# Kernel optimization log

Hardware: AMD Instinct MI355X
Metric: run time of the kernel (lower is better)

Reference implementation:

```python
import jax, jax.numpy as jnp
import numpy as np

LATENT = 1024
ENC = 4096
B = 8192


def setup_inputs() -> dict:
    key = jax.random.key(0)
    k1, k2, k3, k4 = jax.random.split(key, 4)
    inp = jax.random.normal(k1, (B, LATENT), dtype=jnp.float32)
    enc = jax.random.normal(k2, (B, ENC), dtype=jnp.float32)
    # nn.Linear(ENC, LATENT): weight [LATENT, ENC], bias [LATENT]
    bound = 1.0 / np.sqrt(ENC)
    W = jax.random.uniform(k3, (LATENT, ENC), minval=-bound, maxval=bound, dtype=jnp.float32)
    b = jax.random.uniform(k4, (LATENT,), minval=-bound, maxval=bound, dtype=jnp.float32)
    return {"input": inp, "encoder_output": enc, "W": W, "b": b}


def reference(input, encoder_output, W, b):
    # vector = Linear(encoder_output)  -> [B, LATENT]
    v = jnp.einsum("be,de->bd", encoder_output, W) + b
    # Fused Householder-style reflection (math identical to bmm(vv^T, x)):
    # out = x - 2 * v * (v . x) / ||v||   (original divides by norm, not norm^2)
    dot = jnp.sum(v * input, axis=1, keepdims=True)          # [B, 1]
    norm = jnp.linalg.norm(v, axis=1, keepdims=True)         # [B, 1]
    output = input - 2.0 * v * dot / norm                    # [B, LATENT]
    log_det = jnp.zeros((input.shape[0], 1), dtype=input.dtype)
    return (output, log_det)
```

## Files before the change

kernel.cpp:

```cpp
#include <hip/hip_runtime.h>
#include <hip/hip_bf16.h>
#include <stdint.h>

#define M_DIM 8192
#define N_DIM 1024
#define K_DIM 4096

typedef __bf16 bf16x8 __attribute__((ext_vector_type(8)));
typedef float f32x4 __attribute__((ext_vector_type(4)));
typedef __hip_bfloat16 bf16_t;
typedef f32x4 AccT[2][4][2][2];

__device__ __forceinline__ void gload_lds16(const void* g, void* l) {
  __builtin_amdgcn_global_load_lds(
      (const __attribute__((address_space(1))) void*)g,
      (__attribute__((address_space(3))) void*)l, 16, 0, 0);
}

__global__ __launch_bounds__(256) void pack_swz(const float* __restrict__ src,
                                                int4* __restrict__ dst) {
  const unsigned tid = blockIdx.x * 256 + threadIdx.x;
  const unsigned cp = tid & 7;
  const unsigned tmp = tid >> 3;
  const unsigned r = tmp & 255;
  const unsigned tmp2 = tmp >> 8;
  const unsigned kt = tmp2 & 63;
  const unsigned rt = tmp2 >> 6;
  const unsigned srow = (rt << 8) + r;
  const unsigned k0 = (kt << 6) + ((cp ^ (r & 7)) << 3);
  const float4* s = (const float4*)(src + (size_t)srow * 4096 + k0);
  float4 a = s[0], b = s[1];
  union { bf16_t h[8]; int4 v; } u;
  u.h[0] = __float2bfloat16(a.x); u.h[1] = __float2bfloat16(a.y);
  u.h[2] = __float2bfloat16(a.z); u.h[3] = __float2bfloat16(a.w);
  u.h[4] = __float2bfloat16(b.x); u.h[5] = __float2bfloat16(b.y);
  u.h[6] = __float2bfloat16(b.z); u.h[7] = __float2bfloat16(b.w);
  dst[tid] = u.v;
}

__device__ __forceinline__ void stage_half(const char* g, char* smem, int ldsoff, int tid) {
  gload_lds16(g + tid * 16, smem + ldsoff + tid * 16);
  gload_lds16(g + 8192 + tid * 16, smem + ldsoff + 8192 + tid * 16);
}

template <int QM, int QN, int VM>
__device__ __forceinline__ void phase(char* smem, int bb, int wm, int wn,
                                      int lrow, int lkc, int tid,
                                      const char* gsrc, int ldsoff, AccT& acc) {
  bf16x8 af[4][2];
  bf16x8 bfr[2][2];
  const char* ab = smem + bb * 65536;
  #pragma unroll
  for (int f = 0; f < 4; ++f)
    #pragma unroll
    for (int s = 0; s < 2; ++s) {
      int r = QM * 128 + wm * 64 + f * 16 + lrow;
      int c = s * 4 + lkc;
      af[f][s] = *(const bf16x8*)(ab + r * 128 + ((c ^ (r & 7)) << 4));
    }
  #pragma unroll
  for (int f2 = 0; f2 < 2; ++f2)
    #pragma unroll
    for (int s = 0; s < 2; ++s) {
      int r = QN * 128 + wn * 32 + f2 * 16 + lrow;
      int c = s * 4 + lkc;
      bfr[f2][s] = *(const bf16x8*)(ab + 32768 + r * 128 + ((c ^ (r & 7)) << 4));
    }
  stage_half(gsrc, smem, ldsoff, tid);
  __builtin_amdgcn_sched_barrier(0);
  __builtin_amdgcn_s_barrier();
  asm volatile("s_waitcnt lgkmcnt(0)" ::: "memory");
  __builtin_amdgcn_sched_barrier(0);
  __builtin_amdgcn_s_setprio(1);
  #pragma unroll
  for (int f = 0; f < 4; ++f)
    #pragma unroll
    for (int f2 = 0; f2 < 2; ++f2)
      #pragma unroll
      for (int s = 0; s < 2; ++s)
        acc[QM][f][QN][f2] = __builtin_amdgcn_mfma_f32_16x16x32_bf16(
            af[f][s], bfr[f2][s], acc[QM][f][QN][f2], 0, 0, 0);
  __builtin_amdgcn_s_setprio(0);
  if constexpr (VM == 10) asm volatile("s_waitcnt vmcnt(10)" ::: "memory");
  if constexpr (VM == 4)  asm volatile("s_waitcnt vmcnt(4)" ::: "memory");
  __builtin_amdgcn_sched_barrier(0);
  __builtin_amdgcn_s_barrier();
}

__global__ __launch_bounds__(512, 2) void gemm8(
    const char* __restrict__ pA, const char* __restrict__ pB,
    float* __restrict__ V0, float* __restrict__ V1p, int NT) {
  extern __shared__ char smem[];
  const int tid = threadIdx.x;
  const int lane = tid & 63, wave = tid >> 6;
  const int wm = wave >> 2, wn = wave & 3;
  const int lrow = lane & 15, lkc = lane >> 4;

  const int cpx = (int)gridDim.x >> 3;
  const int swz = ((int)blockIdx.x & 7) * cpx + ((int)blockIdx.x >> 3);
  const int split = swz >> 7;
  const int rem = swz & 127;
  const int mt = rem >> 2, nt = rem & 3;

  const char* Abase = pA + ((size_t)mt * 64 + (size_t)split * NT) * 32768;
  const char* Bbase = pB + ((size_t)nt * 64 + (size_t)split * NT) * 32768;
  float* V = split ? V1p : V0;

  AccT acc;
  #pragma unroll
  for (int a0 = 0; a0 < 2; ++a0)
    #pragma unroll
    for (int a1 = 0; a1 < 4; ++a1)
      #pragma unroll
      for (int a2 = 0; a2 < 2; ++a2)
        #pragma unroll
        for (int a3 = 0; a3 < 2; ++a3)
          acc[a0][a1][a2][a3] = (f32x4){0.f, 0.f, 0.f, 0.f};

  const int ktm = NT - 1;

  stage_half(Abase, smem, 0, tid);
  stage_half(Bbase + 16384, smem, 32768 + 16384, tid);
  stage_half(Abase + 16384, smem, 16384, tid);
  stage_half(Bbase, smem, 32768, tid);
  stage_half(Abase + 32768, smem, 65536, tid);
  stage_half(Bbase + 32768 + 16384, smem, 65536 + 32768 + 16384, tid);
  asm volatile("s_waitcnt vmcnt(4)" ::: "memory");
  __builtin_amdgcn_s_barrier();

  for (int g = 0; g < NT; ++g) {
    const int bb = g & 1, nbf = bb ^ 1;
    const char* A1t = Abase + (size_t)((g + 1) & ktm) * 32768;
    const char* B1t = Bbase + (size_t)((g + 1) & ktm) * 32768;
    const char* A2t = Abase + (size_t)((g + 2) & ktm) * 32768;
    const char* B2t = Bbase + (size_t)((g + 2) & ktm) * 32768;
    phase<0, 0, 0>(smem, bb, wm, wn, lrow, lkc, tid, A1t + 16384, nbf * 65536 + 16384, acc);
    phase<0, 1, 10>(smem, bb, wm, wn, lrow, lkc, tid, B1t, nbf * 65536 + 32768, acc);
    phase<1, 1, 0>(smem, bb, wm, wn, lrow, lkc, tid, A2t, bb * 65536, acc);
    phase<1, 0, 4>(smem, bb, wm, wn, lrow, lkc, tid, B2t + 16384, bb * 65536 + 32768 + 16384, acc);
  }

  const int lq = lane >> 4;
  #pragma unroll
  for (int qm = 0; qm < 2; ++qm)
    #pragma unroll
    for (int f = 0; f < 4; ++f)
      #pragma unroll
      for (int qn = 0; qn < 2; ++qn)
        #pragma unroll
        for (int f2 = 0; f2 < 2; ++f2) {
          const int rowg = mt * 256 + qm * 128 + wm * 64 + f * 16 + lq * 4;
          const int colg = nt * 256 + qn * 128 + wn * 32 + f2 * 16 + lrow;
          #pragma unroll
          for (int reg = 0; reg < 4; ++reg)
            V[(size_t)(rowg + reg) * N_DIM + colg] = acc[qm][f][qn][f2][reg];
        }
}

__global__ __launch_bounds__(256) void householder_ep(
    const float* __restrict__ x, const float* __restrict__ bias,
    float* __restrict__ vio, const float* __restrict__ V2,
    float* __restrict__ logdet) {
  const int row = blockIdx.x;
  const int t = threadIdx.x;
  float4* vr = (float4*)(vio + (size_t)row * N_DIM);
  const float4* xr = (const float4*)(x + (size_t)row * N_DIM);
  const float4* br = (const float4*)bias;

  float4 v = vr[t];
  if (V2) {
    float4 v2 = ((const float4*)(V2 + (size_t)row * N_DIM))[t];
    v.x += v2.x; v.y += v2.y; v.z += v2.z; v.w += v2.w;
  }
  float4 bb = br[t];
  v.x += bb.x; v.y += bb.y; v.z += bb.z; v.w += bb.w;
  float4 xx = xr[t];

  float dot = v.x * xx.x + v.y * xx.y + v.z * xx.z + v.w * xx.w;
  float nsq = v.x * v.x + v.y * v.y + v.z * v.z + v.w * v.w;

  #pragma unroll
  for (int off = 32; off > 0; off >>= 1) {
    dot += __shfl_down(dot, off);
    nsq += __shfl_down(nsq, off);
  }
  __shared__ float sd[4], sn[4];
  if ((t & 63) == 0) { sd[t >> 6] = dot; sn[t >> 6] = nsq; }
  __syncthreads();
  dot = sd[0] + sd[1] + sd[2] + sd[3];
  nsq = sn[0] + sn[1] + sn[2] + sn[3];

  const float f = 2.0f * dot / sqrtf(nsq);
  float4 o;
  o.x = xx.x - f * v.x;
  o.y = xx.y - f * v.y;
  o.z = xx.z - f * v.z;
  o.w = xx.w - f * v.w;
  vr[t] = o;
  if (t == 0) logdet[row] = 0.0f;
}

extern "C" void kernel_launch(void* const* d_in, const int* in_sizes, int n_in,
                              void* d_out, int out_size, void* d_ws, size_t ws_size,
                              hipStream_t stream) {
  const float* x   = (const float*)d_in[0];
  const float* enc = (const float*)d_in[1];
  const float* W   = (const float*)d_in[2];
  const float* b   = (const float*)d_in[3];

  float* out    = (float*)d_out;
  float* v      = out;
  float* logdet = out + (size_t)M_DIM * N_DIM;

  char*  packA = (char*)d_ws;
  char*  packB = packA + (size_t)64 * 1024 * 1024;
  float* V2    = (float*)(packB + (size_t)8 * 1024 * 1024);

  const size_t need1 = (size_t)72 * 1024 * 1024;
  const size_t need2 = (size_t)104 * 1024 * 1024;
  const int nsplit = (ws_size >= need2) ? 2 : 1;

  pack_swz<<<(M_DIM * K_DIM / 8) / 256, 256, 0, stream>>>(enc, (int4*)packA);
  pack_swz<<<(N_DIM * K_DIM / 8) / 256, 256, 0, stream>>>(W, (int4*)packB);

  (void)need1;
  hipFuncSetAttribute((const void*)gemm8, hipFuncAttributeMaxDynamicSharedMemorySize, 131072);
  gemm8<<<dim3(128 * nsplit), 512, 131072, stream>>>(
      packA, packB, v, nsplit == 2 ? V2 : nullptr, 64 / nsplit);

  householder_ep<<<M_DIM, 256, 0, stream>>>(x, b, v, nsplit == 2 ? V2 : nullptr, logdet);
}
```

Measured before the change: 134.1 us.

## Reuse LDS fragments across GEMM phases and merge pack kernels

```diff
diff --git a/kernel.cpp b/kernel.cpp
--- a/kernel.cpp
+++ b/kernel.cpp
@@ -9,7 +9,6 @@
 typedef __bf16 bf16x8 __attribute__((ext_vector_type(8)));
 typedef float f32x4 __attribute__((ext_vector_type(4)));
 typedef __hip_bfloat16 bf16_t;
-typedef f32x4 AccT[2][4][2][2];
 
 __device__ __forceinline__ void gload_lds16(const void* g, void* l) {
   __builtin_amdgcn_global_load_lds(
@@ -17,11 +16,18 @@
       (__attribute__((address_space(3))) void*)l, 16, 0, 0);
 }
 
-__global__ __launch_bounds__(256) void pack_swz(const float* __restrict__ src,
-                                                int4* __restrict__ dst) {
-  const unsigned tid = blockIdx.x * 256 + threadIdx.x;
-  const unsigned cp = tid & 7;
-  const unsigned tmp = tid >> 3;
+__global__ __launch_bounds__(256) void pack_both(const float* __restrict__ enc,
+                                                 const float* __restrict__ W,
+                                                 int4* __restrict__ pA,
+                                                 int4* __restrict__ pB) {
+  const unsigned gtid = blockIdx.x * 256 + threadIdx.x;
+  const float* src;
+  int4* dst;
+  unsigned t;
+  if (gtid < 4194304u) { src = enc; dst = pA; t = gtid; }
+  else                 { src = W;   dst = pB; t = gtid - 4194304u; }
+  const unsigned cp = t & 7;
+  const unsigned tmp = t >> 3;
   const unsigned r = tmp & 255;
   const unsigned tmp2 = tmp >> 8;
   const unsigned kt = tmp2 & 63;
@@ -35,56 +41,12 @@
   u.h[2] = __float2bfloat16(a.z); u.h[3] = __float2bfloat16(a.w);
   u.h[4] = __float2bfloat16(b.x); u.h[5] = __float2bfloat16(b.y);
   u.h[6] = __float2bfloat16(b.z); u.h[7] = __float2bfloat16(b.w);
-  dst[tid] = u.v;
+  dst[t] = u.v;
 }
 
 __device__ __forceinline__ void stage_half(const char* g, char* smem, int ldsoff, int tid) {
   gload_lds16(g + tid * 16, smem + ldsoff + tid * 16);
   gload_lds16(g + 8192 + tid * 16, smem + ldsoff + 8192 + tid * 16);
-}
-
-template <int QM, int QN, int VM>
-__device__ __forceinline__ void phase(char* smem, int bb, int wm, int wn,
-                                      int lrow, int lkc, int tid,
-                                      const char* gsrc, int ldsoff, AccT& acc) {
-  bf16x8 af[4][2];
-  bf16x8 bfr[2][2];
-  const char* ab = smem + bb * 65536;
-  #pragma unroll
-  for (int f = 0; f < 4; ++f)
-    #pragma unroll
-    for (int s = 0; s < 2; ++s) {
-      int r = QM * 128 + wm * 64 + f * 16 + lrow;
-      int c = s * 4 + lkc;
-      af[f][s] = *(const bf16x8*)(ab + r * 128 + ((c ^ (r & 7)) << 4));
-    }
-  #pragma unroll
-  for (int f2 = 0; f2 < 2; ++f2)
-    #pragma unroll
-    for (int s = 0; s < 2; ++s) {
-      int r = QN * 128 + wn * 32 + f2 * 16 + lrow;
-      int c = s * 4 + lkc;
-      bfr[f2][s] = *(const bf16x8*)(ab + 32768 + r * 128 + ((c ^ (r & 7)) << 4));
-    }
-  stage_half(gsrc, smem, ldsoff, tid);
-  __builtin_amdgcn_sched_barrier(0);
-  __builtin_amdgcn_s_barrier();
-  asm volatile("s_waitcnt lgkmcnt(0)" ::: "memory");
-  __builtin_amdgcn_sched_barrier(0);
-  __builtin_amdgcn_s_setprio(1);
-  #pragma unroll
-  for (int f = 0; f < 4; ++f)
-    #pragma unroll
-    for (int f2 = 0; f2 < 2; ++f2)
-      #pragma unroll
-      for (int s = 0; s < 2; ++s)
-        acc[QM][f][QN][f2] = __builtin_amdgcn_mfma_f32_16x16x32_bf16(
-            af[f][s], bfr[f2][s], acc[QM][f][QN][f2], 0, 0, 0);
-  __builtin_amdgcn_s_setprio(0);
-  if constexpr (VM == 10) asm volatile("s_waitcnt vmcnt(10)" ::: "memory");
-  if constexpr (VM == 4)  asm volatile("s_waitcnt vmcnt(4)" ::: "memory");
-  __builtin_amdgcn_sched_barrier(0);
-  __builtin_amdgcn_s_barrier();
 }
 
 __global__ __launch_bounds__(512, 2) void gemm8(
@@ -106,7 +68,16 @@
   const char* Bbase = pB + ((size_t)nt * 64 + (size_t)split * NT) * 32768;
   float* V = split ? V1p : V0;
 
-  AccT acc;
+  int colw[2];
+  colw[0] = ((lkc) ^ (lrow & 7)) << 4;
+  colw[1] = ((4 + lkc) ^ (lrow & 7)) << 4;
+  int aRow[4], bRow[2];
+  #pragma unroll
+  for (int f = 0; f < 4; ++f) aRow[f] = (wm * 64 + f * 16 + lrow) * 128;
+  #pragma unroll
+  for (int f2 = 0; f2 < 2; ++f2) bRow[f2] = 32768 + (wn * 32 + f2 * 16 + lrow) * 128;
+
+  f32x4 acc[2][4][2][2];
   #pragma unroll
   for (int a0 = 0; a0 < 2; ++a0)
     #pragma unroll
@@ -130,31 +101,122 @@
 
   for (int g = 0; g < NT; ++g) {
     const int bb = g & 1, nbf = bb ^ 1;
+    char* ab = smem + bb * 65536;
     const char* A1t = Abase + (size_t)((g + 1) & ktm) * 32768;
     const char* B1t = Bbase + (size_t)((g + 1) & ktm) * 32768;
     const char* A2t = Abase + (size_t)((g + 2) & ktm) * 32768;
     const char* B2t = Bbase + (size_t)((g + 2) & ktm) * 32768;
-    phase<0, 0, 0>(smem, bb, wm, wn, lrow, lkc, tid, A1t + 16384, nbf * 65536 + 16384, acc);
-    phase<0, 1, 10>(smem, bb, wm, wn, lrow, lkc, tid, B1t, nbf * 65536 + 32768, acc);
-    phase<1, 1, 0>(smem, bb, wm, wn, lrow, lkc, tid, A2t, bb * 65536, acc);
-    phase<1, 0, 4>(smem, bb, wm, wn, lrow, lkc, tid, B2t + 16384, bb * 65536 + 32768 + 16384, acc);
+
+    bf16x8 a[4][2], b0[2][2], b1[2][2];
+
+    #pragma unroll
+    for (int f = 0; f < 4; ++f)
+      #pragma unroll
+      for (int s = 0; s < 2; ++s)
+        a[f][s] = *(const bf16x8*)(ab + aRow[f] + colw[s]);
+    #pragma unroll
+    for (int f2 = 0; f2 < 2; ++f2)
+      #pragma unroll
+      for (int s = 0; s < 2; ++s)
+        b0[f2][s] = *(const bf16x8*)(ab + bRow[f2] + colw[s]);
+    stage_half(A1t + 16384, smem, nbf * 65536 + 16384, tid);
+    __builtin_amdgcn_sched_barrier(0);
+    __builtin_amdgcn_s_barrier();
+    asm volatile("s_waitcnt lgkmcnt(0)" ::: "memory");
+    __builtin_amdgcn_sched_barrier(0);
+    __builtin_amdgcn_s_setprio(1);
+    #pragma unroll
+    for (int f = 0; f < 4; ++f)
+      #pragma unroll
+      for (int f2 = 0; f2 < 2; ++f2)
+        #pragma unroll
+        for (int s = 0; s < 2; ++s)
+          acc[0][f][0][f2] = __builtin_amdgcn_mfma_f32_16x16x32_bf16(
+              a[f][s], b0[f2][s], acc[0][f][0][f2], 0, 0, 0);
+    __builtin_amdgcn_s_setprio(0);
+    __builtin_amdgcn_sched_barrier(0);
+    __builtin_amdgcn_s_barrier();
+
+    #pragma unroll
+    for (int f2 = 0; f2 < 2; ++f2)
+      #pragma unroll
+      for (int s = 0; s < 2; ++s)
+        b1[f2][s] = *(const bf16x8*)(ab + bRow[f2] + 16384 + colw[s]);
+    stage_half(B1t, smem, nbf * 65536 + 32768, tid);
+    __builtin_amdgcn_sched_barrier(0);
+    __builtin_amdgcn_s_barrier();
+    asm volatile("s_waitcnt lgkmcnt(0)" ::: "memory");
+    __builtin_amdgcn_sched_barrier(0);
+    __builtin_amdgcn_s_setprio(1);
+    #pragma unroll
+    for (int f = 0; f < 4; ++f)
+      #pragma unroll
+      for (int f2 = 0; f2 < 2; ++f2)
+        #pragma unroll
+        for (int s = 0; s < 2; ++s)
+          acc[0][f][1][f2] = __builtin_amdgcn_mfma_f32_16x16x32_bf16(
+              a[f][s], b1[f2][s], acc[0][f][1][f2], 0, 0, 0);
+    __builtin_amdgcn_s_setprio(0);
+    __builtin_amdgcn_sched_barrier(0);
+    __builtin_amdgcn_s_barrier();
+
+    #pragma unroll
+    for (int f = 0; f < 4; ++f)
+      #pragma unroll
+      for (int s = 0; s < 2; ++s)
+        a[f][s] = *(const bf16x8*)(ab + aRow[f] + 16384 + colw[s]);
+    stage_half(A2t, smem, bb * 65536, tid);
+    __builtin_amdgcn_sched_barrier(0);
+    __builtin_amdgcn_s_barrier();
+    asm volatile("s_waitcnt lgkmcnt(0)" ::: "memory");
+    __builtin_amdgcn_sched_barrier(0);
+    __builtin_amdgcn_s_setprio(1);
+    #pragma unroll
+    for (int f = 0; f < 4; ++f)
+      #pragma unroll
+      for (int f2 = 0; f2 < 2; ++f2)
+        #pragma unroll
+        for (int s = 0; s < 2; ++s)
+          acc[1][f][1][f2] = __builtin_amdgcn_mfma_f32_16x16x32_bf16(
+              a[f][s], b1[f2][s], acc[1][f][1][f2], 0, 0, 0);
+    __builtin_amdgcn_s_setprio(0);
+    __builtin_amdgcn_sched_barrier(0);
+    __builtin_amdgcn_s_barrier();
+
+    stage_half(B2t + 16384, smem, bb * 65536 + 32768 + 16384, tid);
+    __builtin_amdgcn_sched_barrier(0);
+    __builtin_amdgcn_s_barrier();
+    __builtin_amdgcn_s_setprio(1);
+    #pragma unroll
+    for (int f = 0; f < 4; ++f)
+      #pragma unroll
+      for (int f2 = 0; f2 < 2; ++f2)
+        #pragma unroll
+        for (int s = 0; s < 2; ++s)
+          acc[1][f][0][f2] = __builtin_amdgcn_mfma_f32_16x16x32_bf16(
+              a[f][s], b0[f2][s], acc[1][f][0][f2], 0, 0, 0);
+    __builtin_amdgcn_s_setprio(0);
+    asm volatile("s_waitcnt vmcnt(4)" ::: "memory");
+    __builtin_amdgcn_sched_barrier(0);
+    __builtin_amdgcn_s_barrier();
   }
 
   const int lq = lane >> 4;
   #pragma unroll
   for (int qm = 0; qm < 2; ++qm)
     #pragma unroll
-    for (int f = 0; f < 4; ++f)
-      #pragma unroll
-      for (int qn = 0; qn < 2; ++qn)
-        #pragma unroll
-        for (int f2 = 0; f2 < 2; ++f2) {
-          const int rowg = mt * 256 + qm * 128 + wm * 64 + f * 16 + lq * 4;
-          const int colg = nt * 256 + qn * 128 + wn * 32 + f2 * 16 + lrow;
+    for (int f = 0; f < 4; ++f) {
+      const int rowg = mt * 256 + qm * 128 + wm * 64 + f * 16 + lq * 4;
+      #pragma unroll
+      for (int reg = 0; reg < 4; ++reg) {
+        float* Vr = V + (size_t)(rowg + reg) * N_DIM + nt * 256 + wn * 32 + lrow;
+        #pragma unroll
+        for (int qn = 0; qn < 2; ++qn)
           #pragma unroll
-          for (int reg = 0; reg < 4; ++reg)
-            V[(size_t)(rowg + reg) * N_DIM + colg] = acc[qm][f][qn][f2][reg];
-        }
+          for (int f2 = 0; f2 < 2; ++f2)
+            Vr[qn * 128 + f2 * 16] = acc[qm][f][qn][f2][reg];
+      }
+    }
 }
 
 __global__ __launch_bounds__(256) void householder_ep(
@@ -216,14 +278,11 @@
   char*  packB = packA + (size_t)64 * 1024 * 1024;
   float* V2    = (float*)(packB + (size_t)8 * 1024 * 1024);
 
-  const size_t need1 = (size_t)72 * 1024 * 1024;
   const size_t need2 = (size_t)104 * 1024 * 1024;
   const int nsplit = (ws_size >= need2) ? 2 : 1;
 
-  pack_swz<<<(M_DIM * K_DIM / 8) / 256, 256, 0, stream>>>(enc, (int4*)packA);
-  pack_swz<<<(N_DIM * K_DIM / 8) / 256, 256, 0, stream>>>(W, (int4*)packB);
-
-  (void)need1;
+  pack_both<<<18432, 256, 0, stream>>>(enc, W, (int4*)packA, (int4*)packB);
+
   hipFuncSetAttribute((const void*)gemm8, hipFuncAttributeMaxDynamicSharedMemorySize, 131072);
   gemm8<<<dim3(128 * nsplit), 512, 131072, stream>>>(
       packA, packB, v, nsplit == 2 ? V2 : nullptr, 64 / nsplit);
```

Measured after the change: 121.9 us. 9.1% less time.
